# Optimization experiments

Measured on AMD Instinct MI355X. Metric: run time of the kernel, lower is better.

The kernel has to match this reference:

```python
import jax, jax.numpy as jnp
from jax import lax
import numpy as np

D = 128          # condition_dim
NUM_STEPS = 1000
FFN = 2048       # torch TransformerEncoderLayer default dim_feedforward


def _conv(x, w, b):
    # 3x3 conv, stride 1, padding 1 (SAME), NCHW / OIHW layout as in torch
    y = lax.conv_general_dilated(x, w, (1, 1), 'SAME',
                                 dimension_numbers=('NCHW', 'OIHW', 'NCHW'))
    return y + b[None, :, None, None]


def _ln(x, g, b):
    m = jnp.mean(x, -1, keepdims=True)
    v = jnp.mean((x - m) ** 2, -1, keepdims=True)
    return (x - m) / jnp.sqrt(v + 1e-5) * g + b


def setup_inputs() -> dict:
    key = jax.random.key(0)
    ks = iter(jax.random.split(key, 40))
    B, C, H, W = 64, 3, 128, 128
    flat = C * H * W
    def rn(shape, scale=0.02):
        return jax.random.normal(next(ks), shape, jnp.float32) * scale
    return dict(
        cond_img=jax.random.normal(next(ks), (B, C, H, W), jnp.float32),
        tgt_img=jax.random.normal(next(ks), (B, C, H, W), jnp.float32),
        noise=jax.random.normal(next(ks), (B, C, H, W), jnp.float32),
        t=jax.random.randint(next(ks), (B,), 0, NUM_STEPS),
        # condition encoder params
        enc_lin_w=rn((D, flat)), enc_lin_b=jnp.zeros((D,), jnp.float32),
        in_w=rn((2, 3 * D, D)), in_b=jnp.zeros((2, 3 * D), jnp.float32),
        out_w=rn((2, D, D)), out_b=jnp.zeros((2, D), jnp.float32),
        ff1_w=rn((2, FFN, D)), ff1_b=jnp.zeros((2, FFN), jnp.float32),
        ff2_w=rn((2, D, FFN)), ff2_b=jnp.zeros((2, D), jnp.float32),
        ln1_g=jnp.ones((2, D), jnp.float32), ln1_b=jnp.zeros((2, D), jnp.float32),
        ln2_g=jnp.ones((2, D), jnp.float32), ln2_b=jnp.zeros((2, D), jnp.float32),
        # SimpleUNet params
        d1_w=rn((32, C, 3, 3)), d1_b=jnp.zeros((32,), jnp.float32),
        d2_w=rn((64, 32, 3, 3)), d2_b=jnp.zeros((64,), jnp.float32),
        mid_w=rn((64, D)), mid_b=jnp.zeros((64,), jnp.float32),
        u1_w=rn((32, 64, 3, 3)), u1_b=jnp.zeros((32,), jnp.float32),
        u2_w=rn((C, 32, 3, 3)), u2_b=jnp.zeros((C,), jnp.float32),
    )


def _forward(cond_img, tgt_img, noise, t,
             enc_lin_w, enc_lin_b, in_w, in_b, out_w, out_b,
             ff1_w, ff1_b, ff2_w, ff2_b, ln1_g, ln1_b, ln2_g, ln2_b,
             d1_w, d1_b, d2_w, d2_b, mid_w, mid_b, u1_w, u1_b, u2_w, u2_b):
    B = cond_img.shape[0]
    # ---- TransformerConditionEncoder (seq_len == 1, eval mode) ----
    x = cond_img.reshape(B, -1) @ enc_lin_w.T + enc_lin_b  # [B, D]
    for i in range(2):
        # self-attention over a length-1 sequence: softmax over one key == 1,
        # so attn(x) == out_proj(v_proj(x)) exactly.
        v = x @ in_w[i][2 * D:3 * D].T + in_b[i][2 * D:3 * D]
        a = v @ out_w[i].T + out_b[i]
        x = _ln(x + a, ln1_g[i], ln1_b[i])
        f = jnp.maximum(x @ ff1_w[i].T + ff1_b[i], 0.0) @ ff2_w[i].T + ff2_b[i]
        x = _ln(x + f, ln2_g[i], ln2_b[i])
    c = x  # [B, D]
    # ---- LinearScheduler.q_sample ----
    betas = jnp.linspace(1e-4, 0.02, NUM_STEPS)
    alpha_bars = jnp.cumprod(1.0 - betas)
    ab = alpha_bars[t][:, None, None, None]
    z_t = jnp.sqrt(ab) * tgt_img + jnp.sqrt(1.0 - ab) * noise
    # ---- SimpleUNet ----
    h = jax.nn.relu(_conv(z_t, d1_w, d1_b))
    h = jax.nn.relu(_conv(h, d2_w, d2_b))
    h = h + (c @ mid_w.T + mid_b)[:, :, None, None]
    h = jax.nn.relu(_conv(h, u1_w, u1_b))
    eps_pred = _conv(h, u2_w, u2_b)
    # ---- MSE loss ----
    return jnp.mean((eps_pred - noise) ** 2)


def reference(cond_img, tgt_img, noise, t,
              enc_lin_w, enc_lin_b, in_w, in_b, out_w, out_b,
              ff1_w, ff1_b, ff2_w, ff2_b, ln1_g, ln1_b, ln2_g, ln2_b,
              d1_w, d1_b, d2_w, d2_b, mid_w, mid_b, u1_w, u1_b, u2_w, u2_b):
    return _forward(cond_img, tgt_img, noise, t,
                    enc_lin_w, enc_lin_b, in_w, in_b, out_w, out_b,
                    ff1_w, ff1_b, ff2_w, ff2_b, ln1_g, ln1_b, ln2_g, ln2_b,
                    d1_w, d1_b, d2_w, d2_b, mid_w, mid_b, u1_w, u1_b, u2_w, u2_b)
```

## Files before the change

kernel.cpp:

```cpp
#include <hip/hip_runtime.h>
#include <math.h>

#define ENC_K 49152
#define KSEG 64
#define KLEN (ENC_K / KSEG)

typedef __attribute__((ext_vector_type(8))) short bf16x8;
typedef __attribute__((ext_vector_type(4))) float f32x4;

__device__ inline unsigned short f2bf(float f) {
    unsigned int u = __builtin_bit_cast(unsigned int, f);
    unsigned int r = u + 0x7fffu + ((u >> 16) & 1u);
    return (unsigned short)(r >> 16);
}
__device__ inline float dot4(const float4 a, const float4 b) {
    return a.x * b.x + a.y * b.y + a.z * b.z + a.w * b.w;
}
__device__ inline unsigned int pk4_fp8(float a, float b, float c, float d) {
    int v = 0;
    v = __builtin_amdgcn_cvt_pk_fp8_f32(a, b, v, false);
    v = __builtin_amdgcn_cvt_pk_fp8_f32(c, d, v, true);
    return (unsigned int)v;
}
__device__ inline f32x4 mfma_fp8(unsigned long long a, unsigned long long b, f32x4 c) {
    return __builtin_amdgcn_mfma_f32_16x16x32_fp8_fp8((long)a, (long)b, c, 0, 0, 0);
}

__device__ inline int xcd_work(int total) {
    int orig = blockIdx.x + gridDim.x * (blockIdx.y + gridDim.y * blockIdx.z);
    return (orig & 7) * (total >> 3) + (orig >> 3);
}

__global__ void k_alpha(const int* __restrict__ t, float* __restrict__ sab, float* __restrict__ snab) {
    int b = threadIdx.x;
    if (b < 64) {
        int tb = t[b];
        const float step = (0.02f - 1e-4f) / 999.0f;
        float ab = 1.0f;
        for (int i = 0; i <= tb; ++i) {
            float beta = 1e-4f + step * (float)i;
            ab *= (1.0f - beta);
        }
        sab[b] = sqrtf(ab);
        snab[b] = sqrtf(1.0f - ab);
    }
}

__global__ void k_prep_cw(const float* __restrict__ w, unsigned short* __restrict__ out, int CO, int CI) {
    int idx = blockIdx.x * 256 + threadIdx.x;
    int total = CO * CI * 9;
    if (idx < total) {
        int tap = idx / (CO * CI);
        int rem = idx % (CO * CI);
        int co = rem / CI, ci = rem % CI;
        out[idx] = f2bf(w[((size_t)co * CI + ci) * 9 + tap]);
    }
}

__global__ void k_prep_u1f8(const float* __restrict__ w, unsigned char* __restrict__ out) {
    int idx = blockIdx.x * 256 + threadIdx.x;
    if (idx < 18432) {
        int tap = idx / 2048, rem = idx % 2048;
        int co = rem >> 6, ci = rem & 63;
        float f = w[((size_t)co * 64 + ci) * 9 + tap];
        int v = __builtin_amdgcn_cvt_pk_fp8_f32(f, 0.f, 0, false);
        out[idx] = (unsigned char)(v & 0xFF);
    }
}

__global__ void k_prep_u2f8(const float* __restrict__ w, unsigned char* __restrict__ out) {
    int idx = blockIdx.x * 256 + threadIdx.x;
    if (idx < 4608) {
        int tap = idx / 512, rem = idx % 512;
        int co = rem >> 5, ci = rem & 31;
        float f = (co < 3) ? w[((size_t)co * 32 + ci) * 9 + tap] : 0.f;
        int v = __builtin_amdgcn_cvt_pk_fp8_f32(f, 0.f, 0, false);
        out[idx] = (unsigned char)(v & 0xFF);
    }
}

__global__ void k_prep_bf(const float* __restrict__ in, unsigned short* __restrict__ out, int n) {
    int i = blockIdx.x * 256 + threadIdx.x;
    if (i < n) out[i] = f2bf(in[i]);
}

__global__ void k_enc_gemm(const float* __restrict__ cond, const float* __restrict__ w,
                           float* __restrict__ partial) {
    __shared__ float As[32][68];
    __shared__ float Ws[32][68];
    int tid = threadIdx.x;
    int j = tid & 15, i = tid >> 4;
    int d0 = blockIdx.x * 32, b0 = blockIdx.y * 32;
    int k0 = blockIdx.z * KLEN;
    float a00 = 0.f, a01 = 0.f, a10 = 0.f, a11 = 0.f;
    for (int kk = 0; kk < KLEN; kk += 64) {
        for (int idx = tid; idx < 512; idx += 256) {
            int r = idx >> 4, c = (idx & 15) << 2;
            *(float4*)&As[r][c] = *(const float4*)&cond[(size_t)(b0 + r) * ENC_K + k0 + kk + c];
            *(float4*)&Ws[r][c] = *(const float4*)&w[(size_t)(d0 + r) * ENC_K + k0 + kk + c];
        }
        __syncthreads();
        const float4* aA = (const float4*)&As[i][0];
        const float4* aB = (const float4*)&As[i + 16][0];
        const float4* wA = (const float4*)&Ws[j][0];
        const float4* wB = (const float4*)&Ws[j + 16][0];
#pragma unroll
        for (int k = 0; k < 16; ++k) {
            float4 av0 = aA[k], av1 = aB[k], wv0 = wA[k], wv1 = wB[k];
            a00 += dot4(av0, wv0); a01 += dot4(av0, wv1);
            a10 += dot4(av1, wv0); a11 += dot4(av1, wv1);
        }
        __syncthreads();
    }
    size_t base = (size_t)blockIdx.z * 64;
    partial[(base + b0 + i) * 128 + d0 + j] = a00;
    partial[(base + b0 + i) * 128 + d0 + j + 16] = a01;
    partial[(base + b0 + i + 16) * 128 + d0 + j] = a10;
    partial[(base + b0 + i + 16) * 128 + d0 + j + 16] = a11;
}

__global__ void k_enc_reduce(const float* __restrict__ partial, const float* __restrict__ bias,
                             float* __restrict__ x0) {
    int idx = blockIdx.x * 256 + threadIdx.x;
    float s = bias[idx & 127];
    for (int ks = 0; ks < KSEG; ++ks) s += partial[(size_t)ks * 8192 + idx];
    x0[idx] = s;
}

__device__ float sum128(float v, int tid, float* red) {
    if (tid < 128) red[tid] = v;
    __syncthreads();
    if (tid < 64) red[tid] += red[tid + 64]; __syncthreads();
    if (tid < 32) red[tid] += red[tid + 32]; __syncthreads();
    if (tid < 16) red[tid] += red[tid + 16]; __syncthreads();
    if (tid < 8)  red[tid] += red[tid + 8];  __syncthreads();
    if (tid < 4)  red[tid] += red[tid + 4];  __syncthreads();
    if (tid < 2)  red[tid] += red[tid + 2];  __syncthreads();
    if (tid < 1)  red[tid] += red[tid + 1];  __syncthreads();
    float s = red[0];
    __syncthreads();
    return s;
}

__global__ __launch_bounds__(512) void k_tf_attn(
    const float* __restrict__ xs, float* __restrict__ yo,
    const float* __restrict__ in_w, const float* __restrict__ in_b,
    const float* __restrict__ out_w, const float* __restrict__ out_b,
    const float* __restrict__ ln1_g, const float* __restrict__ ln1_b, int L) {
    __shared__ float xr[128], vr[128], tp[4][128], red[128];
    int b = blockIdx.x, tid = threadIdx.x;
    if (tid < 128) xr[tid] = xs[b * 128 + tid];
    __syncthreads();
    int d = tid & 127, s = tid >> 7;
    {
        const float4* w = (const float4*)(in_w + ((size_t)L * 384 + 256 + d) * 128) + s * 8;
        const float4* x4 = (const float4*)xr + s * 8;
        float p = 0.f;
#pragma unroll
        for (int k = 0; k < 8; ++k) p += dot4(x4[k], w[k]);
        tp[s][d] = p;
    }
    __syncthreads();
    if (tid < 128) vr[tid] = in_b[L * 384 + 256 + tid] + tp[0][tid] + tp[1][tid] + tp[2][tid] + tp[3][tid];
    __syncthreads();
    {
        const float4* w = (const float4*)(out_w + ((size_t)L * 128 + d) * 128) + s * 8;
        const float4* v4 = (const float4*)vr + s * 8;
        float p = 0.f;
#pragma unroll
        for (int k = 0; k < 8; ++k) p += dot4(v4[k], w[k]);
        tp[s][d] = p;
    }
    __syncthreads();
    float y = 0.f;
    if (tid < 128) y = xr[tid] + out_b[L * 128 + tid] + tp[0][tid] + tp[1][tid] + tp[2][tid] + tp[3][tid];
    float m1 = sum128(y, tid, red) * (1.f / 128.f);
    float c1 = y - m1;
    float v1 = sum128(c1 * c1, tid, red) * (1.f / 128.f);
    if (tid < 128)
        yo[b * 128 + tid] = c1 * rsqrtf(v1 + 1e-5f) * ln1_g[L * 128 + tid] + ln1_b[L * 128 + tid];
}

__global__ __launch_bounds__(256, 2) void k_ff1m(
    const float* __restrict__ yo, const unsigned short* __restrict__ w1b,
    const float* __restrict__ ff1_b, unsigned short* __restrict__ f1, int L) {
    __shared__ __align__(16) unsigned short xs[64 * 136];
    int tid = threadIdx.x;
    int lane = tid & 63, wv = tid >> 6, l15 = lane & 15, ch = lane >> 4;
    int n0 = blockIdx.x * 64 + wv * 16;
    for (int e = tid; e < 8192; e += 256)
        xs[(e >> 7) * 136 + (e & 127)] = f2bf(yo[e]);
    __syncthreads();
    f32x4 acc[4];
    f32x4 zf = {0.f, 0.f, 0.f, 0.f};
#pragma unroll
    for (int rg = 0; rg < 4; ++rg) acc[rg] = zf;
    const unsigned short* wrow = w1b + ((size_t)L * 2048 + n0 + l15) * 128 + ch * 8;
#pragma unroll
    for (int ks = 0; ks < 4; ++ks) {
        bf16x8 af = *(const bf16x8*)(wrow + ks * 32);
#pragma unroll
        for (int rg = 0; rg < 4; ++rg) {
            bf16x8 bv = *(const bf16x8*)(xs + (rg * 16 + l15) * 136 + ks * 32 + ch * 8);
            acc[rg] = __builtin_amdgcn_mfma_f32_16x16x32_bf16(af, bv, acc[rg], 0, 0, 0);
        }
    }
#pragma unroll
    for (int rg = 0; rg < 4; ++rg) {
        ushort4 o;
#pragma unroll
        for (int r = 0; r < 4; ++r)
            ((unsigned short*)&o)[r] =
                f2bf(fmaxf(acc[rg][r] + ff1_b[L * 2048 + n0 + ch * 4 + r], 0.f));
        *(ushort4*)(f1 + (size_t)(rg * 16 + l15) * 2056 + n0 + ch * 4) = o;
    }
}

__global__ __launch_bounds__(256, 2) void k_ff2m(
    const unsigned short* __restrict__ f1, const unsigned short* __restrict__ w2b,
    float* __restrict__ part, int L) {
    int tid = threadIdx.x;
    int lane = tid & 63, wv = tid >> 6, l15 = lane & 15, ch = lane >> 4;
    int ks = blockIdx.x;
    int dw = blockIdx.y * 64 + wv * 16;
    f32x4 acc[4];
    f32x4 zf = {0.f, 0.f, 0.f, 0.f};
#pragma unroll
    for (int rg = 0; rg < 4; ++rg) acc[rg] = zf;
    const unsigned short* wrow = w2b + ((size_t)L * 128 + dw + l15) * 2048 + ks * 512 + ch * 8;
    const unsigned short* frow = f1 + ks * 512 + ch * 8;
#pragma unroll
    for (int kst = 0; kst < 16; ++kst) {
        bf16x8 af = *(const bf16x8*)(wrow + kst * 32);
#pragma unroll
        for (int rg = 0; rg < 4; ++rg) {
            bf16x8 bv = *(const bf16x8*)(frow + (size_t)(rg * 16 + l15) * 2056 + kst * 32);
            acc[rg] = __builtin_amdgcn_mfma_f32_16x16x32_bf16(af, bv, acc[rg], 0, 0, 0);
        }
    }
#pragma unroll
    for (int rg = 0; rg < 4; ++rg)
        *(float4*)&part[((size_t)ks * 64 + rg * 16 + l15) * 128 + dw + ch * 4] = *(float4*)&acc[rg];
}

__global__ __launch_bounds__(128) void k_tf_red(
    const float* __restrict__ part, const float* __restrict__ yo,
    float* __restrict__ xs, const float* __restrict__ ff2_b,
    const float* __restrict__ ln2_g, const float* __restrict__ ln2_b, int L) {
    __shared__ float red[128];
    int b = blockIdx.x, tid = threadIdx.x;
    float y2 = yo[b * 128 + tid] + ff2_b[L * 128 + tid];
#pragma unroll
    for (int ks = 0; ks < 4; ++ks) y2 += part[((size_t)ks * 64 + b) * 128 + tid];
    float m2 = sum128(y2, tid, red) * (1.f / 128.f);
    float c2 = y2 - m2;
    float v2 = sum128(c2 * c2, tid, red) * (1.f / 128.f);
    xs[b * 128 + tid] = c2 * rsqrtf(v2 + 1e-5f) * ln2_g[L * 128 + tid] + ln2_b[L * 128 + tid];
}

__global__ void k_mid(const float* __restrict__ xe, const float* __restrict__ mid_w,
                      const float* __restrict__ mid_b, float* __restrict__ mid) {
    int b = blockIdx.x, c = threadIdx.x;
    float s = mid_b[c];
    const float* xr = xe + b * 128;
    const float* wr = mid_w + c * 128;
    for (int k = 0; k < 128; ++k) s += xr[k] * wr[k];
    mid[b * 64 + c] = s;
}

__global__ __launch_bounds__(256, 4) void k_conv1(
    const float* __restrict__ tgt, const float* __restrict__ noise,
    const float* __restrict__ sab, const float* __restrict__ snab,
    const float* __restrict__ wgt, const float* __restrict__ bias,
    unsigned short* __restrict__ h1, int b0) {
    __shared__ float it[3][18][35];
    __shared__ float wt[16][3][9];
    int tid = threadIdx.x;
    int tx = tid & 15, ty = tid >> 4;
    int total = gridDim.x * gridDim.y * gridDim.z;
    int w = xcd_work(total);
    int bx = w % gridDim.x; int t2 = w / gridDim.x;
    int by = t2 % gridDim.y; int bz = t2 / gridDim.y;
    int bl = bz >> 1, g = bz & 1;
    int bg = b0 + bl, co0 = g * 16;
    float za = sab[bg], zb = snab[bg];
    for (int idx = tid; idx < 3 * 18 * 34; idx += 256) {
        int c = idx / (18 * 34), rem = idx % (18 * 34);
        int yy = rem / 34, xx = rem % 34;
        int gy = by * 16 + yy - 1, gx = bx * 32 + xx - 1;
        float v = 0.f;
        if (gy >= 0 && gy < 128 && gx >= 0 && gx < 128) {
            size_t off = (((size_t)bg * 3 + c) * 128 + gy) * 128 + gx;
            v = za * tgt[off] + zb * noise[off];
        }
        it[c][yy][xx] = v;
    }
    for (int idx = tid; idx < 16 * 27; idx += 256) {
        int co = idx / 27, rem = idx % 27;
        wt[co][rem / 9][rem % 9] = wgt[(size_t)(co0 + co) * 27 + rem];
    }
    __syncthreads();
    float acc[16][2];
#pragma unroll
    for (int co = 0; co < 16; ++co) { acc[co][0] = 0.f; acc[co][1] = 0.f; }
#pragma unroll
    for (int c = 0; c < 3; ++c)
#pragma unroll
        for (int ky = 0; ky < 3; ++ky) {
            float win[4];
#pragma unroll
            for (int i = 0; i < 4; ++i) win[i] = it[c][ty + ky][tx * 2 + i];
#pragma unroll
            for (int kx = 0; kx < 3; ++kx)
#pragma unroll
                for (int co = 0; co < 16; ++co) {
                    float ww = wt[co][c][ky * 3 + kx];
                    acc[co][0] += win[kx] * ww;
                    acc[co][1] += win[kx + 1] * ww;
                }
        }
    int gy = by * 16 + ty, gx0 = bx * 32 + tx * 2;
#pragma unroll
    for (int p = 0; p < 2; ++p) {
        __attribute__((aligned(16))) unsigned short ov[16];
#pragma unroll
        for (int co = 0; co < 16; ++co)
            ov[co] = f2bf(fmaxf(acc[co][p] + bias[co0 + co], 0.f));
        size_t o = (((size_t)bl * 128 + gy) * 128 + gx0 + p) * 32 + co0;
        *(float4*)(h1 + o) = *(float4*)&ov[0];
        *(float4*)(h1 + o + 8) = *(float4*)&ov[8];
    }
}

template <int CIN, int COB, int COUT, int MOUT, int OF8>
__global__ __launch_bounds__(256, 2) void k_convMg(
    const unsigned short* __restrict__ in, const unsigned short* __restrict__ wb,
    const float* __restrict__ bias, const float* __restrict__ mid,
    unsigned short* __restrict__ out, int b0) {
    const int GROUPS = COUT / (16 * COB);
    __shared__ __align__(16) unsigned short in_t[10 * 34 * 40];
    __shared__ __align__(16) unsigned short w_t[9 * COB * 16 * 40];
    int tid = threadIdx.x;
    int total = gridDim.x * gridDim.y * gridDim.z;
    int wk = xcd_work(total);
    int bx = wk % gridDim.x; int t2 = wk / gridDim.x;
    int by = t2 % gridDim.y; int bz = t2 / gridDim.y;
    int bl = bz / GROUPS, g = bz % GROUPS;
    int bg = b0 + bl;
    int co0 = g * COB * 16;
    int lane = tid & 63, wv = tid >> 6;
    int l15 = lane & 15, ch = lane >> 4;

    f32x4 acc[2][2][COB];
    f32x4 zf = {0.f, 0.f, 0.f, 0.f};
#pragma unroll
    for (int a = 0; a < 2; ++a)
#pragma unroll
        for (int bq = 0; bq < 2; ++bq)
#pragma unroll
            for (int c = 0; c < COB; ++c) acc[a][bq][c] = zf;

    for (int cs = 0; cs < CIN / 32; ++cs) {
        if (cs) __syncthreads();
        for (int c = tid; c < 10 * 34 * 4; c += 256) {
            int cc = c & 3, pix = c >> 2;
            int xx = pix % 34, yy = pix / 34;
            int gy = by * 8 + yy - 1, gx = bx * 32 + xx - 1;
            bf16x8 v = {0, 0, 0, 0, 0, 0, 0, 0};
            if (gy >= 0 && gy < 128 && gx >= 0 && gx < 128)
                v = *(const bf16x8*)(in + (((size_t)bl * 128 + gy) * 128 + gx) * CIN + cs * 32 + cc * 8);
            *(bf16x8*)(in_t + pix * 40 + cc * 8) = v;
        }
        for (int c = tid; c < 9 * COB * 16 * 4; c += 256) {
            int cc = c & 3, row = c >> 2;
            int tap = row / (COB * 16), co = row % (COB * 16);
            bf16x8 v = *(const bf16x8*)(wb + ((size_t)(tap * COUT + co0 + co)) * CIN + cs * 32 + cc * 8);
            *(bf16x8*)(w_t + row * 40 + cc * 8) = v;
        }
        __syncthreads();
#pragma unroll
        for (int ky = 0; ky < 3; ++ky)
#pragma unroll
            for (int kx = 0; kx < 3; ++kx) {
                int tap = ky * 3 + kx;
                bf16x8 af[COB];
#pragma unroll
                for (int cb = 0; cb < COB; ++cb)
                    af[cb] = *(const bf16x8*)(w_t + (tap * COB * 16 + cb * 16 + l15) * 40 + ch * 8);
#pragma unroll
                for (int yl = 0; yl < 2; ++yl) {
                    int yloc = 2 * wv + yl + ky;
#pragma unroll
                    for (int xt = 0; xt < 2; ++xt) {
                        int xloc = xt * 16 + l15 + kx;
                        bf16x8 bfv = *(const bf16x8*)(in_t + (yloc * 34 + xloc) * 40 + ch * 8);
#pragma unroll
                        for (int cb = 0; cb < COB; ++cb)
                            acc[yl][xt][cb] = __builtin_amdgcn_mfma_f32_16x16x32_bf16(
                                af[cb], bfv, acc[yl][xt][cb], 0, 0, 0);
                    }
                }
            }
    }
#pragma unroll
    for (int yl = 0; yl < 2; ++yl) {
        int gy = by * 8 + 2 * wv + yl;
#pragma unroll
        for (int xt = 0; xt < 2; ++xt) {
            int gx = bx * 32 + xt * 16 + l15;
            size_t pixo = (((size_t)bl * 128 + gy) * 128 + gx) * COUT;
#pragma unroll
            for (int cb = 0; cb < COB; ++cb) {
                int co = co0 + cb * 16 + ch * 4;
                float vv[4];
#pragma unroll
                for (int r = 0; r < 4; ++r) {
                    float v = acc[yl][xt][cb][r] + bias[co + r];
                    v = fmaxf(v, 0.f);
                    if (MOUT == 2) v += mid[bg * 64 + co + r];
                    vv[r] = v;
                }
                if (OF8) {
                    unsigned int pk = pk4_fp8(vv[0], vv[1], vv[2], vv[3]);
                    *(unsigned int*)((unsigned char*)out + pixo + co) = pk;
                } else {
                    ushort4 o;
#pragma unroll
                    for (int r = 0; r < 4; ++r) ((unsigned short*)&o)[r] = f2bf(vv[r]);
                    *(ushort4*)(out + pixo + co) = o;
                }
            }
        }
    }
}

__global__ __launch_bounds__(256, 3) void k_convF8u1(
    const unsigned char* __restrict__ h2, const unsigned char* __restrict__ wb,
    const float* __restrict__ bias, unsigned char* __restrict__ h3, int b0) {
    __shared__ __align__(16) unsigned char in_t[340 * 72];
    __shared__ __align__(16) unsigned char w_t[288 * 72];
    int tid = threadIdx.x;
    int total = gridDim.x * gridDim.y * gridDim.z;
    int wk = xcd_work(total);
    int bx = wk % gridDim.x; int t2 = wk / gridDim.x;
    int by = t2 % gridDim.y; int bl = t2 / gridDim.y;
    int lane = tid & 63, wv = tid >> 6, l15 = lane & 15, ch = lane >> 4;

    for (int c = tid; c < 340 * 8; c += 256) {
        int cc = c & 7, pix = c >> 3;
        int xx = pix % 34, yy = pix / 34;
        int gy = by * 8 + yy - 1, gx = bx * 32 + xx - 1;
        unsigned long long v = 0ull;
        if (gy >= 0 && gy < 128 && gx >= 0 && gx < 128)
            v = *(const unsigned long long*)(h2 + (((size_t)bl * 128 + gy) * 128 + gx) * 64 + cc * 8);
        *(unsigned long long*)(in_t + pix * 72 + cc * 8) = v;
    }
    for (int c = tid; c < 288 * 8; c += 256) {
        int cc = c & 7, row = c >> 3;
        *(unsigned long long*)(w_t + row * 72 + cc * 8) =
            *(const unsigned long long*)(wb + (size_t)row * 64 + cc * 8);
    }
    __syncthreads();

    f32x4 acc[2][2][2];
    f32x4 zf = {0.f, 0.f, 0.f, 0.f};
#pragma unroll
    for (int a = 0; a < 2; ++a)
#pragma unroll
        for (int bq = 0; bq < 2; ++bq)
#pragma unroll
            for (int c = 0; c < 2; ++c) acc[a][bq][c] = zf;

#pragma unroll
    for (int cs = 0; cs < 2; ++cs)
#pragma unroll
        for (int ky = 0; ky < 3; ++ky)
#pragma unroll
            for (int kx = 0; kx < 3; ++kx) {
                int tap = ky * 3 + kx;
                unsigned long long A[2];
#pragma unroll
                for (int cb = 0; cb < 2; ++cb)
                    A[cb] = *(const unsigned long long*)(
                        w_t + (tap * 32 + cb * 16 + l15) * 72 + cs * 32 + ch * 8);
#pragma unroll
                for (int yl = 0; yl < 2; ++yl) {
                    int yloc = 2 * wv + yl + ky;
#pragma unroll
                    for (int xt = 0; xt < 2; ++xt) {
                        int xloc = xt * 16 + l15 + kx;
                        unsigned long long B = *(const unsigned long long*)(
                            in_t + (yloc * 34 + xloc) * 72 + cs * 32 + ch * 8);
#pragma unroll
                        for (int cb = 0; cb < 2; ++cb)
                            acc[yl][xt][cb] = mfma_fp8(A[cb], B, acc[yl][xt][cb]);
                    }
                }
            }
#pragma unroll
    for (int yl = 0; yl < 2; ++yl) {
        int gy = by * 8 + 2 * wv + yl;
#pragma unroll
        for (int xt = 0; xt < 2; ++xt) {
            int gx = bx * 32 + xt * 16 + l15;
            size_t pixo = (((size_t)bl * 128 + gy) * 128 + gx) * 32;
#pragma unroll
            for (int cb = 0; cb < 2; ++cb) {
                int co = cb * 16 + ch * 4;
                float v0 = fmaxf(acc[yl][xt][cb][0] + bias[co], 0.f);
                float v1 = fmaxf(acc[yl][xt][cb][1] + bias[co + 1], 0.f);
                float v2 = fmaxf(acc[yl][xt][cb][2] + bias[co + 2], 0.f);
                float v3 = fmaxf(acc[yl][xt][cb][3] + bias[co + 3], 0.f);
                *(unsigned int*)(h3 + pixo + co) = pk4_fp8(v0, v1, v2, v3);
            }
        }
    }
}

__global__ __launch_bounds__(256, 3) void k_u2f8(
    const unsigned char* __restrict__ h3, const unsigned char* __restrict__ wbu2,
    const float* __restrict__ u2_b, const float* __restrict__ noise,
    float* __restrict__ partial, int b0) {
    __shared__ __align__(16) unsigned char in_t[340 * 40];
    __shared__ __align__(16) unsigned char w_t[144 * 40];
    __shared__ float rs[256];
    int tid = threadIdx.x;
    int total = gridDim.x * gridDim.y * gridDim.z;
    int wk = xcd_work(total);
    int bx = wk % gridDim.x; int t2 = wk / gridDim.x;
    int by = t2 % gridDim.y; int bl = t2 / gridDim.y;
    int bg = b0 + bl;
    int lane = tid & 63, wv = tid >> 6, l15 = lane & 15, ch = lane >> 4;

    for (int c = tid; c < 340 * 4; c += 256) {
        int cc = c & 3, pix = c >> 2;
        int xx = pix % 34, yy = pix / 34;
        int gy = by * 8 + yy - 1, gx = bx * 32 + xx - 1;
        unsigned long long v = 0ull;
        if (gy >= 0 && gy < 128 && gx >= 0 && gx < 128)
            v = *(const unsigned long long*)(h3 + (((size_t)bl * 128 + gy) * 128 + gx) * 32 + cc * 8);
        *(unsigned long long*)(in_t + pix * 40 + cc * 8) = v;
    }
    for (int c = tid; c < 144 * 4; c += 256) {
        int cc = c & 3, row = c >> 2;
        *(unsigned long long*)(w_t + row * 40 + cc * 8) =
            *(const unsigned long long*)(wbu2 + (size_t)row * 32 + cc * 8);
    }
    __syncthreads();

    f32x4 acc[2][2];
    f32x4 zf = {0.f, 0.f, 0.f, 0.f};
    acc[0][0] = zf; acc[0][1] = zf; acc[1][0] = zf; acc[1][1] = zf;
#pragma unroll
    for (int ky = 0; ky < 3; ++ky)
#pragma unroll
        for (int kx = 0; kx < 3; ++kx) {
            int tap = ky * 3 + kx;
            unsigned long long A = *(const unsigned long long*)(
                w_t + (tap * 16 + l15) * 40 + ch * 8);
#pragma unroll
            for (int yl = 0; yl < 2; ++yl) {
                int yloc = 2 * wv + yl + ky;
#pragma unroll
                for (int xt = 0; xt < 2; ++xt) {
                    int xloc = xt * 16 + l15 + kx;
                    unsigned long long B = *(const unsigned long long*)(
                        in_t + (yloc * 34 + xloc) * 40 + ch * 8);
                    acc[yl][xt] = mfma_fp8(A, B, acc[yl][xt]);
                }
            }
        }
    float ss = 0.f;
    if (ch == 0) {
#pragma unroll
        for (int yl = 0; yl < 2; ++yl) {
            int gy = by * 8 + 2 * wv + yl;
#pragma unroll
            for (int xt = 0; xt < 2; ++xt) {
                int gx = bx * 32 + xt * 16 + l15;
#pragma unroll
                for (int r = 0; r < 3; ++r) {
                    float v = acc[yl][xt][r] + u2_b[r];
                    float d = v - noise[(((size_t)bg * 3 + r) * 128 + gy) * 128 + gx];
                    ss += d * d;
                }
            }
        }
    }
    rs[tid] = ss;
    __syncthreads();
    for (int s = 128; s > 0; s >>= 1) {
        if (tid < s) rs[tid] += rs[tid + s];
        __syncthreads();
    }
    if (tid == 0) partial[bg * 64 + by * 4 + bx] = rs[0];
}

__global__ void k_final(const float* __restrict__ partial, float* __restrict__ out) {
    __shared__ float rs[256];
    int tid = threadIdx.x;
    float s = 0.f;
    for (int i = tid; i < 4096; i += 256) s += partial[i];
    rs[tid] = s;
    __syncthreads();
    for (int st = 128; st > 0; st >>= 1) {
        if (tid < st) rs[tid] += rs[tid + st];
        __syncthreads();
    }
    if (tid == 0) out[0] = rs[0] / 3145728.0f;
}

extern "C" void kernel_launch(void* const* d_in, const int* in_sizes, int n_in,
                              void* d_out, int out_size, void* d_ws, size_t ws_size,
                              hipStream_t stream) {
    const float* cond   = (const float*)d_in[0];
    const float* tgt    = (const float*)d_in[1];
    const float* noise  = (const float*)d_in[2];
    const int*   t      = (const int*)d_in[3];
    const float* enc_w  = (const float*)d_in[4];
    const float* enc_b  = (const float*)d_in[5];
    const float* in_w   = (const float*)d_in[6];
    const float* in_b   = (const float*)d_in[7];
    const float* out_w  = (const float*)d_in[8];
    const float* out_b  = (const float*)d_in[9];
    const float* ff1_w  = (const float*)d_in[10];
    const float* ff1_b  = (const float*)d_in[11];
    const float* ff2_w  = (const float*)d_in[12];
    const float* ff2_b  = (const float*)d_in[13];
    const float* ln1_g  = (const float*)d_in[14];
    const float* ln1_b  = (const float*)d_in[15];
    const float* ln2_g  = (const float*)d_in[16];
    const float* ln2_b  = (const float*)d_in[17];
    const float* d1_w   = (const float*)d_in[18];
    const float* d1_b   = (const float*)d_in[19];
    const float* d2_w   = (const float*)d_in[20];
    const float* d2_b   = (const float*)d_in[21];
    const float* mid_w  = (const float*)d_in[22];
    const float* mid_b  = (const float*)d_in[23];
    const float* u1_w   = (const float*)d_in[24];
    const float* u1_b   = (const float*)d_in[25];
    const float* u2_w   = (const float*)d_in[26];
    const float* u2_b   = (const float*)d_in[27];

    float* ws = (float*)d_ws;
    float* sab     = ws;
    float* snab    = ws + 64;
    float* x0      = ws + 128;
    float* mid     = ws + 16512;
    float* msepart = ws + 86144;
    unsigned short* wb2   = (unsigned short*)(ws + 90240);
    unsigned char*  wbu1f = (unsigned char*)(ws + 99456);
    unsigned char*  wbu2f = (unsigned char*)(ws + 108672);

    const size_t SMALL = 131072;
    const size_t ENCP = (size_t)KSEG * 8192;
    float* encpart = ws + SMALL;
    float* tfy     = encpart + ENCP;
    unsigned short* tff1 = (unsigned short*)(tfy + 8192);
    float* tfpart  = tfy + 8192 + 65792;
    unsigned short* wbf1 = (unsigned short*)(tfpart + 32768);
    unsigned short* wbf2 = (unsigned short*)(tfpart + 32768 + 262144);

    size_t fixed = SMALL + ENCP + 8192 + 65792 + 32768 + 262144 + 262144;
    size_t avail = (ws_size / 4 > fixed) ? (ws_size / 4 - fixed) : 0;
    int NB = 1;
    const int cands[7] = {64, 32, 16, 8, 4, 2, 1};
    for (int ci = 0; ci < 7; ++ci) {
        if ((size_t)cands[ci] * 655360ull <= avail) { NB = cands[ci]; break; }
    }
    unsigned short* hb1 = (unsigned short*)(ws + fixed);
    unsigned char*  hb2 = (unsigned char*)(ws + fixed + (size_t)NB * 262144ull);
    unsigned char*  hb3 = (unsigned char*)(ws + fixed + (size_t)NB * 524288ull);

    k_alpha<<<1, 64, 0, stream>>>(t, sab, snab);
    k_prep_cw<<<72, 256, 0, stream>>>(d2_w, wb2, 64, 32);
    k_prep_u1f8<<<72, 256, 0, stream>>>(u1_w, wbu1f);
    k_prep_u2f8<<<18, 256, 0, stream>>>(u2_w, wbu2f);
    k_prep_bf<<<2048, 256, 0, stream>>>(ff1_w, wbf1, 524288);
    k_prep_bf<<<2048, 256, 0, stream>>>(ff2_w, wbf2, 524288);
    k_enc_gemm<<<dim3(4, 2, KSEG), 256, 0, stream>>>(cond, enc_w, encpart);
    k_enc_reduce<<<32, 256, 0, stream>>>(encpart, enc_b, x0);
    for (int L = 0; L < 2; ++L) {
        k_tf_attn<<<64, 512, 0, stream>>>(x0, tfy, in_w, in_b, out_w, out_b, ln1_g, ln1_b, L);
        k_ff1m<<<32, 256, 0, stream>>>(tfy, wbf1, ff1_b, tff1, L);
        k_ff2m<<<dim3(4, 2), 256, 0, stream>>>(tff1, wbf2, tfpart, L);
        k_tf_red<<<64, 128, 0, stream>>>(tfpart, tfy, x0, ff2_b, ln2_g, ln2_b, L);
    }
    k_mid<<<64, 64, 0, stream>>>(x0, mid_w, mid_b, mid);

    for (int cb = 0; cb < 64; cb += NB) {
        k_conv1<<<dim3(4, 8, NB * 2), 256, 0, stream>>>(
            tgt, noise, sab, snab, d1_w, d1_b, hb1, cb);
        k_convMg<32, 4, 64, 2, 1><<<dim3(4, 16, NB), 256, 0, stream>>>(
            hb1, wb2, d2_b, mid, (unsigned short*)hb2, cb);
        k_convF8u1<<<dim3(4, 16, NB), 256, 0, stream>>>(
            hb2, wbu1f, u1_b, hb3, cb);
        k_u2f8<<<dim3(4, 16, NB), 256, 0, stream>>>(
            hb3, wbu2f, u2_b, noise, msepart, cb);
    }

    k_final<<<1, 256, 0, stream>>>(msepart, (float*)d_out);
}
```

Baseline: 401.0 us.

## Restructure conv1 per-pixel tiling and stage conv outputs through LDS for coalesced stores

conv1 now has each block compute all 32 output channels for an 8x32 tile, one pixel per thread, instead of splitting channels into two groups with two pixels per thread. That removes the duplicated input staging and the redundant alpha-blend work across the channel groups. conv2 becomes a specialized non-templated kernel for 32->64 channels with fp8 output. Both conv2 and u1 now write their fp8 results into shared memory first, then copy them out with contiguous 16-byte stores per pixel, which should coalesce global writes better at the cost of extra barriers and LDS traffic.

```diff
diff --git a/kernel.cpp b/kernel.cpp
--- a/kernel.cpp
+++ b/kernel.cpp
@@ -273,21 +273,20 @@
     const float* __restrict__ sab, const float* __restrict__ snab,
     const float* __restrict__ wgt, const float* __restrict__ bias,
     unsigned short* __restrict__ h1, int b0) {
-    __shared__ float it[3][18][35];
-    __shared__ float wt[16][3][9];
-    int tid = threadIdx.x;
-    int tx = tid & 15, ty = tid >> 4;
+    __shared__ float it[3][10][35];
+    __shared__ float wt[32][27];
+    int tid = threadIdx.x;
     int total = gridDim.x * gridDim.y * gridDim.z;
-    int w = xcd_work(total);
-    int bx = w % gridDim.x; int t2 = w / gridDim.x;
-    int by = t2 % gridDim.y; int bz = t2 / gridDim.y;
-    int bl = bz >> 1, g = bz & 1;
-    int bg = b0 + bl, co0 = g * 16;
+    int wk = xcd_work(total);
+    int bx = wk % gridDim.x; int t2 = wk / gridDim.x;
+    int by = t2 % gridDim.y; int bl = t2 / gridDim.y;
+    int bg = b0 + bl;
+    int px = tid & 31, py = tid >> 5;
     float za = sab[bg], zb = snab[bg];
-    for (int idx = tid; idx < 3 * 18 * 34; idx += 256) {
-        int c = idx / (18 * 34), rem = idx % (18 * 34);
+    for (int idx = tid; idx < 3 * 10 * 34; idx += 256) {
+        int c = idx / 340, rem = idx % 340;
         int yy = rem / 34, xx = rem % 34;
-        int gy = by * 16 + yy - 1, gx = bx * 32 + xx - 1;
+        int gy = by * 8 + yy - 1, gx = bx * 32 + xx - 1;
         float v = 0.f;
         if (gy >= 0 && gy < 128 && gx >= 0 && gx < 128) {
             size_t off = (((size_t)bg * 3 + c) * 128 + gy) * 128 + gx;
@@ -295,143 +294,123 @@
         }
         it[c][yy][xx] = v;
     }
-    for (int idx = tid; idx < 16 * 27; idx += 256) {
-        int co = idx / 27, rem = idx % 27;
-        wt[co][rem / 9][rem % 9] = wgt[(size_t)(co0 + co) * 27 + rem];
-    }
-    __syncthreads();
-    float acc[16][2];
-#pragma unroll
-    for (int co = 0; co < 16; ++co) { acc[co][0] = 0.f; acc[co][1] = 0.f; }
+    for (int idx = tid; idx < 32 * 27; idx += 256)
+        wt[idx / 27][idx % 27] = wgt[idx];
+    __syncthreads();
+    float acc[32];
+#pragma unroll
+    for (int co = 0; co < 32; ++co) acc[co] = 0.f;
 #pragma unroll
     for (int c = 0; c < 3; ++c)
 #pragma unroll
-        for (int ky = 0; ky < 3; ++ky) {
-            float win[4];
-#pragma unroll
-            for (int i = 0; i < 4; ++i) win[i] = it[c][ty + ky][tx * 2 + i];
-#pragma unroll
-            for (int kx = 0; kx < 3; ++kx)
-#pragma unroll
-                for (int co = 0; co < 16; ++co) {
-                    float ww = wt[co][c][ky * 3 + kx];
-                    acc[co][0] += win[kx] * ww;
-                    acc[co][1] += win[kx + 1] * ww;
-                }
-        }
-    int gy = by * 16 + ty, gx0 = bx * 32 + tx * 2;
-#pragma unroll
-    for (int p = 0; p < 2; ++p) {
-        __attribute__((aligned(16))) unsigned short ov[16];
-#pragma unroll
-        for (int co = 0; co < 16; ++co)
-            ov[co] = f2bf(fmaxf(acc[co][p] + bias[co0 + co], 0.f));
-        size_t o = (((size_t)bl * 128 + gy) * 128 + gx0 + p) * 32 + co0;
-        *(float4*)(h1 + o) = *(float4*)&ov[0];
-        *(float4*)(h1 + o + 8) = *(float4*)&ov[8];
-    }
-}
-
-template <int CIN, int COB, int COUT, int MOUT, int OF8>
-__global__ __launch_bounds__(256, 2) void k_convMg(
+        for (int ky = 0; ky < 3; ++ky)
+#pragma unroll
+            for (int kx = 0; kx < 3; ++kx) {
+                float iv = it[c][py + ky][px + kx];
+                int k = c * 9 + ky * 3 + kx;
+#pragma unroll
+                for (int co = 0; co < 32; ++co) acc[co] += iv * wt[co][k];
+            }
+    int gy = by * 8 + py, gx = bx * 32 + px;
+    __attribute__((aligned(16))) unsigned short ov[32];
+#pragma unroll
+    for (int co = 0; co < 32; ++co)
+        ov[co] = f2bf(fmaxf(acc[co] + bias[co], 0.f));
+    size_t o = (((size_t)bl * 128 + gy) * 128 + gx) * 32;
+    float4* dst = (float4*)(h1 + o);
+    const float4* src = (const float4*)ov;
+    dst[0] = src[0]; dst[1] = src[1]; dst[2] = src[2]; dst[3] = src[3];
+}
+
+__global__ __launch_bounds__(256, 2) void k_conv2(
     const unsigned short* __restrict__ in, const unsigned short* __restrict__ wb,
     const float* __restrict__ bias, const float* __restrict__ mid,
-    unsigned short* __restrict__ out, int b0) {
-    const int GROUPS = COUT / (16 * COB);
+    unsigned char* __restrict__ out, int b0) {
     __shared__ __align__(16) unsigned short in_t[10 * 34 * 40];
-    __shared__ __align__(16) unsigned short w_t[9 * COB * 16 * 40];
+    __shared__ __align__(16) unsigned short w_t[9 * 64 * 40];
     int tid = threadIdx.x;
     int total = gridDim.x * gridDim.y * gridDim.z;
     int wk = xcd_work(total);
     int bx = wk % gridDim.x; int t2 = wk / gridDim.x;
-    int by = t2 % gridDim.y; int bz = t2 / gridDim.y;
-    int bl = bz / GROUPS, g = bz % GROUPS;
+    int by = t2 % gridDim.y; int bl = t2 / gridDim.y;
     int bg = b0 + bl;
-    int co0 = g * COB * 16;
     int lane = tid & 63, wv = tid >> 6;
     int l15 = lane & 15, ch = lane >> 4;
 
-    f32x4 acc[2][2][COB];
+    f32x4 acc[2][2][4];
     f32x4 zf = {0.f, 0.f, 0.f, 0.f};
 #pragma unroll
     for (int a = 0; a < 2; ++a)
 #pragma unroll
         for (int bq = 0; bq < 2; ++bq)
 #pragma unroll
-            for (int c = 0; c < COB; ++c) acc[a][bq][c] = zf;
-
-    for (int cs = 0; cs < CIN / 32; ++cs) {
-        if (cs) __syncthreads();
-        for (int c = tid; c < 10 * 34 * 4; c += 256) {
-            int cc = c & 3, pix = c >> 2;
-            int xx = pix % 34, yy = pix / 34;
-            int gy = by * 8 + yy - 1, gx = bx * 32 + xx - 1;
-            bf16x8 v = {0, 0, 0, 0, 0, 0, 0, 0};
-            if (gy >= 0 && gy < 128 && gx >= 0 && gx < 128)
-                v = *(const bf16x8*)(in + (((size_t)bl * 128 + gy) * 128 + gx) * CIN + cs * 32 + cc * 8);
-            *(bf16x8*)(in_t + pix * 40 + cc * 8) = v;
-        }
-        for (int c = tid; c < 9 * COB * 16 * 4; c += 256) {
-            int cc = c & 3, row = c >> 2;
-            int tap = row / (COB * 16), co = row % (COB * 16);
-            bf16x8 v = *(const bf16x8*)(wb + ((size_t)(tap * COUT + co0 + co)) * CIN + cs * 32 + cc * 8);
-            *(bf16x8*)(w_t + row * 40 + cc * 8) = v;
-        }
-        __syncthreads();
-#pragma unroll
-        for (int ky = 0; ky < 3; ++ky)
-#pragma unroll
-            for (int kx = 0; kx < 3; ++kx) {
-                int tap = ky * 3 + kx;
-                bf16x8 af[COB];
-#pragma unroll
-                for (int cb = 0; cb < COB; ++cb)
-                    af[cb] = *(const bf16x8*)(w_t + (tap * COB * 16 + cb * 16 + l15) * 40 + ch * 8);
-#pragma unroll
-                for (int yl = 0; yl < 2; ++yl) {
-                    int yloc = 2 * wv + yl + ky;
-#pragma unroll
-                    for (int xt = 0; xt < 2; ++xt) {
-                        int xloc = xt * 16 + l15 + kx;
-                        bf16x8 bfv = *(const bf16x8*)(in_t + (yloc * 34 + xloc) * 40 + ch * 8);
-#pragma unroll
-                        for (int cb = 0; cb < COB; ++cb)
-                            acc[yl][xt][cb] = __builtin_amdgcn_mfma_f32_16x16x32_bf16(
-                                af[cb], bfv, acc[yl][xt][cb], 0, 0, 0);
-                    }
+            for (int c = 0; c < 4; ++c) acc[a][bq][c] = zf;
+
+    for (int c = tid; c < 10 * 34 * 4; c += 256) {
+        int cc = c & 3, pix = c >> 2;
+        int xx = pix % 34, yy = pix / 34;
+        int gy = by * 8 + yy - 1, gx = bx * 32 + xx - 1;
+        bf16x8 v = {0, 0, 0, 0, 0, 0, 0, 0};
+        if (gy >= 0 && gy < 128 && gx >= 0 && gx < 128)
+            v = *(const bf16x8*)(in + (((size_t)bl * 128 + gy) * 128 + gx) * 32 + cc * 8);
+        *(bf16x8*)(in_t + pix * 40 + cc * 8) = v;
+    }
+    for (int c = tid; c < 9 * 64 * 4; c += 256) {
+        int cc = c & 3, row = c >> 2;
+        bf16x8 v = *(const bf16x8*)(wb + (size_t)row * 32 + cc * 8);
+        *(bf16x8*)(w_t + row * 40 + cc * 8) = v;
+    }
+    __syncthreads();
+#pragma unroll
+    for (int ky = 0; ky < 3; ++ky)
+#pragma unroll
+        for (int kx = 0; kx < 3; ++kx) {
+            int tap = ky * 3 + kx;
+            bf16x8 af[4];
+#pragma unroll
+            for (int cb = 0; cb < 4; ++cb)
+                af[cb] = *(const bf16x8*)(w_t + (tap * 64 + cb * 16 + l15) * 40 + ch * 8);
+#pragma unroll
+            for (int yl = 0; yl < 2; ++yl) {
+                int yloc = 2 * wv + yl + ky;
+#pragma unroll
+                for (int xt = 0; xt < 2; ++xt) {
+                    int xloc = xt * 16 + l15 + kx;
+                    bf16x8 bfv = *(const bf16x8*)(in_t + (yloc * 34 + xloc) * 40 + ch * 8);
+#pragma unroll
+                    for (int cb = 0; cb < 4; ++cb)
+                        acc[yl][xt][cb] = __builtin_amdgcn_mfma_f32_16x16x32_bf16(
+                            af[cb], bfv, acc[yl][xt][cb], 0, 0, 0);
                 }
             }
-    }
-#pragma unroll
-    for (int yl = 0; yl < 2; ++yl) {
-        int gy = by * 8 + 2 * wv + yl;
+        }
+    __syncthreads();
+    unsigned char* st = (unsigned char*)w_t;
+#pragma unroll
+    for (int yl = 0; yl < 2; ++yl)
 #pragma unroll
         for (int xt = 0; xt < 2; ++xt) {
-            int gx = bx * 32 + xt * 16 + l15;
-            size_t pixo = (((size_t)bl * 128 + gy) * 128 + gx) * COUT;
-#pragma unroll
-            for (int cb = 0; cb < COB; ++cb) {
-                int co = co0 + cb * 16 + ch * 4;
+            int pixl = (2 * wv + yl) * 32 + xt * 16 + l15;
+#pragma unroll
+            for (int cb = 0; cb < 4; ++cb) {
+                int co = cb * 16 + ch * 4;
                 float vv[4];
 #pragma unroll
                 for (int r = 0; r < 4; ++r) {
                     float v = acc[yl][xt][cb][r] + bias[co + r];
                     v = fmaxf(v, 0.f);
-                    if (MOUT == 2) v += mid[bg * 64 + co + r];
+                    v += mid[bg * 64 + co + r];
                     vv[r] = v;
                 }
-                if (OF8) {
-                    unsigned int pk = pk4_fp8(vv[0], vv[1], vv[2], vv[3]);
-                    *(unsigned int*)((unsigned char*)out + pixo + co) = pk;
-                } else {
-                    ushort4 o;
-#pragma unroll
-                    for (int r = 0; r < 4; ++r) ((unsigned short*)&o)[r] = f2bf(vv[r]);
-                    *(ushort4*)(out + pixo + co) = o;
-                }
+                *(unsigned int*)(st + pixl * 64 + co) = pk4_fp8(vv[0], vv[1], vv[2], vv[3]);
             }
         }
-    }
+    __syncthreads();
+    int r = tid >> 5, cidx = tid & 31;
+    size_t gb = (((size_t)bl * 128 + by * 8 + r) * 128 + bx * 32 + cidx) * 64;
+    const float4* src = (const float4*)(st + tid * 64);
+    float4* dst = (float4*)(out + gb);
+    dst[0] = src[0]; dst[1] = src[1]; dst[2] = src[2]; dst[3] = src[3];
 }
 
 __global__ __launch_bounds__(256, 3) void k_convF8u1(
@@ -497,13 +476,13 @@
                     }
                 }
             }
-#pragma unroll
-    for (int yl = 0; yl < 2; ++yl) {
-        int gy = by * 8 + 2 * wv + yl;
+    __syncthreads();
+    unsigned char* st = w_t;
+#pragma unroll
+    for (int yl = 0; yl < 2; ++yl)
 #pragma unroll
         for (int xt = 0; xt < 2; ++xt) {
-            int gx = bx * 32 + xt * 16 + l15;
-            size_t pixo = (((size_t)bl * 128 + gy) * 128 + gx) * 32;
+            int pixl = (2 * wv + yl) * 32 + xt * 16 + l15;
 #pragma unroll
             for (int cb = 0; cb < 2; ++cb) {
                 int co = cb * 16 + ch * 4;
@@ -511,10 +490,15 @@
                 float v1 = fmaxf(acc[yl][xt][cb][1] + bias[co + 1], 0.f);
                 float v2 = fmaxf(acc[yl][xt][cb][2] + bias[co + 2], 0.f);
                 float v3 = fmaxf(acc[yl][xt][cb][3] + bias[co + 3], 0.f);
-                *(unsigned int*)(h3 + pixo + co) = pk4_fp8(v0, v1, v2, v3);
+                *(unsigned int*)(st + pixl * 32 + co) = pk4_fp8(v0, v1, v2, v3);
             }
         }
-    }
+    __syncthreads();
+    int r = tid >> 5, cidx = tid & 31;
+    size_t gb = (((size_t)bl * 128 + by * 8 + r) * 128 + bx * 32 + cidx) * 32;
+    const float4* src = (const float4*)(st + tid * 32);
+    float4* dst = (float4*)(h3 + gb);
+    dst[0] = src[0]; dst[1] = src[1];
 }
 
 __global__ __launch_bounds__(256, 3) void k_u2f8(
@@ -689,10 +673,10 @@
     k_mid<<<64, 64, 0, stream>>>(x0, mid_w, mid_b, mid);
 
     for (int cb = 0; cb < 64; cb += NB) {
-        k_conv1<<<dim3(4, 8, NB * 2), 256, 0, stream>>>(
+        k_conv1<<<dim3(4, 16, NB), 256, 0, stream>>>(
             tgt, noise, sab, snab, d1_w, d1_b, hb1, cb);
-        k_convMg<32, 4, 64, 2, 1><<<dim3(4, 16, NB), 256, 0, stream>>>(
-            hb1, wb2, d2_b, mid, (unsigned short*)hb2, cb);
+        k_conv2<<<dim3(4, 16, NB), 256, 0, stream>>>(
+            hb1, wb2, d2_b, mid, hb2, cb);
         k_convF8u1<<<dim3(4, 16, NB), 256, 0, stream>>>(
             hb2, wbu1f, u1_b, hb3, cb);
         k_u2f8<<<dim3(4, 16, NB), 256, 0, stream>>>(
```

Result: slower. 416.1 us (+3.7%).
